# Kernel tuning notes

Hardware: AMD Instinct MI355X
Metric: run time of the kernel (lower is better)

The kernel has to match this reference:

```python
import jax, jax.numpy as jnp
import numpy as np
import math

H = 12
D_MODEL = 768
D_K = D_MODEL // H


def setup_inputs() -> dict:
    key = jax.random.key(0)
    ks = jax.random.split(key, 12)
    B, L = 128, 512
    s = 1.0 / math.sqrt(D_MODEL)
    return {
        "Q": jax.random.normal(ks[0], (B, L, D_MODEL), jnp.float32),
        "K": jax.random.normal(ks[1], (B, L, D_MODEL), jnp.float32),
        "V": jax.random.normal(ks[2], (B, L, D_MODEL), jnp.float32),
        "mask": jax.random.uniform(ks[3], (B, B), jnp.float32),
        "Wq": jax.random.normal(ks[4], (D_MODEL, D_MODEL), jnp.float32) * s,
        "bq": jnp.zeros((D_MODEL,), jnp.float32),
        "Wk": jax.random.normal(ks[5], (D_MODEL, D_MODEL), jnp.float32) * s,
        "bk": jnp.zeros((D_MODEL,), jnp.float32),
        "Wv": jax.random.normal(ks[6], (D_MODEL, D_MODEL), jnp.float32) * s,
        "bv": jnp.zeros((D_MODEL,), jnp.float32),
        "Wo": jax.random.normal(ks[7], (D_MODEL, D_MODEL), jnp.float32) * s,
        "bo": jnp.zeros((D_MODEL,), jnp.float32),
    }


def reference(Q, K, V, mask, Wq, bq, Wk, bk, Wv, bv, Wo, bo):
    nb_q = Q.shape[0]   # nbatches_q = Q.size(0) in the torch code
    nb_kv = K.shape[0]
    # Linear projections then the module's exact reshape/transpose pattern.
    q = (Q @ Wq + bq).reshape(-1, nb_q, H, D_K).swapaxes(1, 2)   # (L, h, B, d_k)
    k = (K @ Wk + bk).reshape(-1, nb_kv, H, D_K).swapaxes(1, 2)  # (L, h, B, d_k)
    v = (V @ Wv + bv).reshape(-1, nb_kv, H, D_K).swapaxes(1, 2)  # (L, h, B, d_k)
    # AttentionAgger: model_dim = d_k -> scale by sqrt(d_k)
    attn = jnp.einsum('lhbd,lhed->lhbe', q, k) / math.sqrt(D_K)  # (L, h, B, B)
    # dual softmax with additive mask bias (mask scaled by its leading dim)
    m = jax.nn.softmax(mask / mask.shape[0], axis=-1)            # (B, B), broadcasts
    attn = jax.nn.softmax(attn, axis=-1) + m
    attn = jax.nn.softmax(attn, axis=-1)
    x = jnp.einsum('lhbe,lhed->lhbd', attn, v)                   # (L, h, B, d_k)
    x = x.swapaxes(1, 2).reshape(-1, nb_q, H * D_K)              # (L, B, d_model)
    return x @ Wo + bo
```

## Files before the change

### kernel.cpp

```cpp
#include <hip/hip_runtime.h>


typedef __attribute__((ext_vector_type(8))) __bf16 bf16x8;
typedef __attribute__((ext_vector_type(4))) __bf16 bf16x4;
typedef __attribute__((ext_vector_type(4))) float f32x4;

#define DM 768
#define LOG2E 1.44269504f

__device__ __forceinline__ unsigned short f2bf(float x) {
  unsigned u = __float_as_uint(x);
  u += 0x7FFFu + ((u >> 16) & 1u);
  return (unsigned short)(u >> 16);
}

__device__ __forceinline__ void gl_lds16(const void* g, void* l) {
  __builtin_amdgcn_global_load_lds(
      (const __attribute__((address_space(1))) unsigned int*)g,
      (__attribute__((address_space(3))) unsigned int*)l, 16, 0, 0);
}

__global__ __launch_bounds__(256) void prep_w(const float* __restrict__ w0,
                                              const float* __restrict__ w1,
                                              const float* __restrict__ w2,
                                              const float* __restrict__ w3,
                                              unsigned short* __restrict__ wt) {
  __shared__ float t[32][33];
  const int op = blockIdx.z;
  const float* w = (op == 0) ? w0 : (op == 1) ? w1 : (op == 2) ? w2 : w3;
  unsigned short* o = wt + (size_t)op * DM * DM;
  const int n0 = blockIdx.x * 32, k0 = blockIdx.y * 32;
  const int tx = threadIdx.x & 31, ty = threadIdx.x >> 5;
#pragma unroll
  for (int r = 0; r < 4; ++r)
    t[r * 8 + ty][tx] = w[(size_t)(k0 + r * 8 + ty) * DM + n0 + tx];
  __syncthreads();
#pragma unroll
  for (int r = 0; r < 4; ++r)
    o[(size_t)(n0 + r * 8 + ty) * DM + k0 + tx] = f2bf(t[tx][r * 8 + ty]);
}

__global__ void prep_m(const float* __restrict__ mask, float* __restrict__ mm) {
  int row = blockIdx.x;
  int t = threadIdx.x;
  float a = mask[row * 128 + t] * (1.0f / 128.0f);
  float b = mask[row * 128 + t + 64] * (1.0f / 128.0f);
  float mx = fmaxf(a, b);
  for (int s = 1; s < 64; s <<= 1) mx = fmaxf(mx, __shfl_xor(mx, s));
  float ea = __expf(a - mx), eb = __expf(b - mx);
  float sum = ea + eb;
  for (int s = 1; s < 64; s <<= 1) sum += __shfl_xor(sum, s);
  float inv = LOG2E / sum;
  mm[row * 128 + t] = ea * inv;
  mm[row * 128 + t + 64] = eb * inv;
}

__global__ __launch_bounds__(256) void convb(const float* __restrict__ in,
                                             unsigned short* __restrict__ out, int n8) {
  int i = blockIdx.x * 256 + threadIdx.x;
  const int stride = gridDim.x * 256;
  for (; i < n8; i += stride) {
    const float4 a = ((const float4*)in)[(size_t)i * 2];
    const float4 b = ((const float4*)in)[(size_t)i * 2 + 1];
    ushort4 lo = {f2bf(a.x), f2bf(a.y), f2bf(a.z), f2bf(a.w)};
    ushort4 hi = {f2bf(b.x), f2bf(b.y), f2bf(b.z), f2bf(b.w)};
    ((ushort4*)out)[(size_t)i * 2] = lo;
    ((ushort4*)out)[(size_t)i * 2 + 1] = hi;
  }
}

__device__ __forceinline__ void stage_tile(const unsigned short* __restrict__ src,
                                           int row0, int kcol, char* slotbase, int tid) {
  const int wid = tid >> 6, lane = tid & 63;
#pragma unroll
  for (int s = 0; s < 2; ++s) {
    const int row = s * 128 + wid * 16 + (lane >> 2);
    const int slot = lane & 3;
    gl_lds16(src + (size_t)(row0 + row) * DM + kcol + ((slot ^ ((row >> 1) & 3)) * 8),
             slotbase + s * 8192 + wid * 1024);
  }
}

template <bool OUT_BF16>
__global__ __launch_bounds__(512, 2) void gemm8(const unsigned short* __restrict__ A,
                                                const unsigned short* __restrict__ Bt,
                                                const float* __restrict__ bias,
                                                void* __restrict__ Outp) {
  __shared__ char smem[131072];
  const int tid = threadIdx.x, lane = tid & 63, wid = tid >> 6;
  const int cl = lane & 15, g = lane >> 4;
  const int wm = wid >> 2, wn = wid & 3;
  const int bid = blockIdx.x;
  const int xcd = bid & 7, bi = bid >> 3;
  const int m0 = (xcd * 32 + bi / 3) * 256;
  const int n0 = (bi % 3) * 256;

  f32x4 acc[8][4] = {};

  auto aslot = [&](int t) { return (char*)smem + (t & 3) * 16384; };
  auto bslot = [&](int t) { return (char*)smem + 65536 + (t & 3) * 16384; };

  auto lda = [&](bf16x8* af, int t, int half) {
#pragma unroll
    for (int mi = 0; mi < 4; ++mi) {
      const int r = wm * 128 + (half * 4 + mi) * 16 + cl;
      af[mi] = *(const bf16x8*)(aslot(t) + r * 64 + ((g ^ ((r >> 1) & 3)) * 16));
    }
  };
  auto ldb = [&](bf16x8* bf, int t) {
#pragma unroll
    for (int ni = 0; ni < 4; ++ni) {
      const int r = wn * 64 + ni * 16 + cl;
      bf[ni] = *(const bf16x8*)(bslot(t) + r * 64 + ((g ^ ((r >> 1) & 3)) * 16));
    }
  };
  auto mfma16 = [&](bf16x8* af, bf16x8* bf, int half) {
    __builtin_amdgcn_s_setprio(1);
#pragma unroll
    for (int mi = 0; mi < 4; ++mi)
#pragma unroll
      for (int ni = 0; ni < 4; ++ni)
        acc[half * 4 + mi][ni] = __builtin_amdgcn_mfma_f32_16x16x32_bf16(
            af[mi], bf[ni], acc[half * 4 + mi][ni], 0, 0, 0);
    __builtin_amdgcn_s_setprio(0);
  };

  auto stg2 = [&](int u) {
    stage_tile(A, m0, u * 32, aslot(u), tid);
    stage_tile(Bt, n0, u * 32, bslot(u), tid);
  };

  stg2(0); stg2(1);
  asm volatile("s_waitcnt vmcnt(0)" ::: "memory");
  __builtin_amdgcn_s_barrier();

  bf16x8 afA[4], af1[4], afB[4], bfA[4], bfB[4];

#pragma unroll 1
  for (int t = 0; t < 12; ++t) {
    const int u = 2 * t;
    if (t < 11) {
      stg2(u + 2); stg2(u + 3);
      asm volatile("s_waitcnt vmcnt(8)" ::: "memory");
    } else {
      asm volatile("s_waitcnt vmcnt(0)" ::: "memory");
    }
    __builtin_amdgcn_s_barrier();
    lda(afA, u, 0); ldb(bfA, u);
    lda(af1, u, 1);
    mfma16(afA, bfA, 0);
    lda(afB, u + 1, 0); ldb(bfB, u + 1);
    mfma16(af1, bfA, 1);
    lda(afA, u + 1, 1);
    mfma16(afB, bfB, 0);
    mfma16(afA, bfB, 1);
    __builtin_amdgcn_s_barrier();
  }

  float bb[4];
#pragma unroll
  for (int ni = 0; ni < 4; ++ni) bb[ni] = bias[n0 + wn * 64 + ni * 16 + cl];
#pragma unroll
  for (int mi = 0; mi < 8; ++mi) {
    const int row = m0 + wm * 128 + mi * 16 + g * 4;
#pragma unroll
    for (int ni = 0; ni < 4; ++ni) {
      const int col = n0 + wn * 64 + ni * 16 + cl;
#pragma unroll
      for (int e = 0; e < 4; ++e) {
        float v = acc[mi][ni][e] + bb[ni];
        if constexpr (OUT_BF16)
          ((unsigned short*)Outp)[(size_t)(row + e) * DM + col] = f2bf(v);
        else
          ((float*)Outp)[(size_t)(row + e) * DM + col] = v;
      }
    }
  }
}

__global__ __launch_bounds__(512) void attn_k(const unsigned short* __restrict__ qp,
                                              const unsigned short* __restrict__ kp,
                                              const unsigned short* __restrict__ vp,
                                              const float* __restrict__ mm,
                                              unsigned short* __restrict__ xout) {
  __shared__ char smem[32768];
  unsigned short* vt = (unsigned short*)(smem + 16384);

  const int tid = threadIdx.x, lane = tid & 63, wid = tid >> 6;
  const int cl = lane & 15, g = lane >> 4;
  const int h = blockIdx.x, l = blockIdx.y;
  const size_t base = (size_t)l * 128 * DM + h * 64;
  const int q = wid * 16 + cl;

#pragma unroll
  for (int p = 0; p < 2; ++p) {
    const int chunk = p * 8 + wid;
    const int row = chunk * 8 + (lane >> 3);
    const int gi = (lane & 7) ^ (row & 7);
    gl_lds16(kp + base + (size_t)row * DM + gi * 8, smem + chunk * 1024);
  }
  if (tid < 256) {
    const int dc = (tid & 7) * 8;
    const int kq = tid >> 3;
    const int pg = (kq ^ ((tid & 7) << 2));
    int4 r0 = *(const int4*)&vp[base + (size_t)(kq * 4 + 0) * DM + dc];
    int4 r1 = *(const int4*)&vp[base + (size_t)(kq * 4 + 1) * DM + dc];
    int4 r2 = *(const int4*)&vp[base + (size_t)(kq * 4 + 2) * DM + dc];
    int4 r3 = *(const int4*)&vp[base + (size_t)(kq * 4 + 3) * DM + dc];
    const unsigned short* u0 = (const unsigned short*)&r0;
    const unsigned short* u1 = (const unsigned short*)&r1;
    const unsigned short* u2 = (const unsigned short*)&r2;
    const unsigned short* u3 = (const unsigned short*)&r3;
#pragma unroll
    for (int j = 0; j < 8; ++j) {
      ushort4 w = {u0[j], u1[j], u2[j], u3[j]};
      *(ushort4*)&vt[(dc + j) * 128 + pg * 4] = w;
    }
  }
  bf16x8 qf[2];
#pragma unroll
  for (int ksr = 0; ksr < 2; ++ksr)
    qf[ksr] = *(const bf16x8*)&qp[base + (size_t)q * DM + ksr * 32 + g * 8];
  __syncthreads();

  f32x4 sacc[8] = {};
  __builtin_amdgcn_s_setprio(1);
#pragma unroll
  for (int ksr = 0; ksr < 2; ++ksr) {
#pragma unroll
    for (int kf = 0; kf < 8; ++kf) {
      const int row = kf * 16 + cl;
      const int gi = (ksr * 4 + g) ^ (row & 7);
      bf16x8 kfr = *(const bf16x8*)(smem + row * 128 + gi * 16);
      sacc[kf] = __builtin_amdgcn_mfma_f32_16x16x32_bf16(kfr, qf[ksr], sacc[kf], 0, 0, 0);
    }
  }
  __builtin_amdgcn_s_setprio(0);
  __syncthreads();

  bf16x4 pk[8];
  {
    float4 mrow[8];
#pragma unroll
    for (int kf = 0; kf < 8; ++kf)
      mrow[kf] = *(const float4*)&mm[q * 128 + kf * 16 + g * 4];
    float sm = 0.f;
#pragma unroll
    for (int kf = 0; kf < 8; ++kf)
#pragma unroll
      for (int e = 0; e < 4; ++e) {
        float p = exp2f(sacc[kf][e] * (0.125f * LOG2E));
        sacc[kf][e] = p;
        sm += p;
      }
    sm += __shfl_xor(sm, 16); sm += __shfl_xor(sm, 32);
    const float inv2e = LOG2E / sm;
    float s2 = 0.f;
#pragma unroll
    for (int kf = 0; kf < 8; ++kf)
#pragma unroll
      for (int e = 0; e < 4; ++e) {
        float p = exp2f(fmaf(sacc[kf][e], inv2e, ((const float*)&mrow[kf])[e]));
        sacc[kf][e] = p;
        s2 += p;
      }
    s2 += __shfl_xor(s2, 16); s2 += __shfl_xor(s2, 32);
    const float inv2 = 1.0f / s2;
#pragma unroll
    for (int kf = 0; kf < 8; ++kf)
      pk[kf] = {(__bf16)(sacc[kf][0] * inv2), (__bf16)(sacc[kf][1] * inv2),
                (__bf16)(sacc[kf][2] * inv2), (__bf16)(sacc[kf][3] * inv2)};
  }

  f32x4 xacc[4] = {};
#pragma unroll
  for (int half = 0; half < 2; ++half) {
#pragma unroll
    for (int kf = 0; kf < 4; ++kf) {
      const int gi = (kf * 4 + g) ^ ((q & 3) << 2);
      *(bf16x4*)(smem + q * 128 + gi * 8) = pk[half * 4 + kf];
    }
    asm volatile("s_waitcnt lgkmcnt(0)" ::: "memory");
    __builtin_amdgcn_sched_barrier(0);
    __builtin_amdgcn_s_setprio(1);
#pragma unroll
    for (int k2 = 0; k2 < 2; ++k2) {
      const int ks2 = half * 2 + k2;
      const int gi = (k2 * 8 + g * 2) ^ ((q & 3) << 2);
      bf16x8 pa = *(const bf16x8*)(smem + q * 128 + gi * 8);
#pragma unroll
      for (int fc = 0; fc < 4; ++fc) {
        const int d = fc * 16 + cl;
        const int pg = (ks2 * 8 + 2 * g) ^ (((d >> 3) & 7) << 2);
        bf16x8 bv = *(const bf16x8*)&vt[d * 128 + pg * 4];
        xacc[fc] = __builtin_amdgcn_mfma_f32_16x16x32_bf16(pa, bv, xacc[fc], 0, 0, 0);
      }
    }
    __builtin_amdgcn_s_setprio(0);
    if (half == 0) {
      asm volatile("s_waitcnt lgkmcnt(0)" ::: "memory");
      __builtin_amdgcn_sched_barrier(0);
    }
  }

#pragma unroll
  for (int fc = 0; fc < 4; ++fc)
#pragma unroll
    for (int e = 0; e < 4; ++e) {
      const int qr = wid * 16 + g * 4 + e;
      __bf16 b = (__bf16)xacc[fc][e];
      unsigned short u;
      __builtin_memcpy(&u, &b, 2);
      xout[base + (size_t)qr * DM + fc * 16 + cl] = u;
    }
}

extern "C" void kernel_launch(void* const* d_in, const int* in_sizes, int n_in,
                              void* d_out, int out_size, void* d_ws, size_t ws_size,
                              hipStream_t stream) {
  (void)in_sizes; (void)n_in; (void)out_size; (void)ws_size;
  const float* Q = (const float*)d_in[0];
  const float* K = (const float*)d_in[1];
  const float* V = (const float*)d_in[2];
  const float* mask = (const float*)d_in[3];
  const float* Wq = (const float*)d_in[4];
  const float* bq = (const float*)d_in[5];
  const float* Wk = (const float*)d_in[6];
  const float* bk = (const float*)d_in[7];
  const float* Wv = (const float*)d_in[8];
  const float* bv = (const float*)d_in[9];
  const float* Wo = (const float*)d_in[10];
  const float* bo = (const float*)d_in[11];

  const size_t NP = (size_t)65536 * DM;

  unsigned short* qp = (unsigned short*)d_out;
  unsigned short* kp = qp + NP;
  unsigned short* S1 = (unsigned short*)d_ws;
  unsigned short* S2 = S1 + NP;
  unsigned short* wt = S2 + NP;
  float* mm = (float*)(wt + (size_t)4 * DM * DM);

  prep_w<<<dim3(24, 24, 4), 256, 0, stream>>>(Wq, Wk, Wv, Wo, wt);
  prep_m<<<dim3(128), 64, 0, stream>>>(mask, mm);

  const int n8 = (int)(NP / 8);
  dim3 g8(768);

  convb<<<dim3(2048), 256, 0, stream>>>(Q, S1, n8);
  gemm8<true><<<g8, 512, 0, stream>>>(S1, wt + 0 * (size_t)DM * DM, bq, qp);
  convb<<<dim3(2048), 256, 0, stream>>>(K, S1, n8);
  gemm8<true><<<g8, 512, 0, stream>>>(S1, wt + 1 * (size_t)DM * DM, bk, kp);
  convb<<<dim3(2048), 256, 0, stream>>>(V, S2, n8);
  gemm8<true><<<g8, 512, 0, stream>>>(S2, wt + 2 * (size_t)DM * DM, bv, S1);

  attn_k<<<dim3(12, 512), 512, 0, stream>>>(qp, kp, S1, mm, S1);

  gemm8<false><<<g8, 512, 0, stream>>>(S1, wt + 3 * (size_t)DM * DM, bo, (float*)d_out);
}
```

Measured before the change: 734.4 us.

## Restructure GEMM main loop into fine-grained 8-phase ping-pong schedule

Replaces the GEMM K-loop, which staged two 32-wide K tiles at a time and then ran four MFMA blocks, with a schedule that handles 64-wide K tiles in two ping-pong LDS buffers. Each iteration is split into eight phases separated by barriers. Each phase interleaves LDS fragment reads, the next tile's global-to-LDS loads for half of A or all of B, and a 4x2x2 MFMA block. The goal is to hide global load latency and LDS reads behind MFMA work, in the style of hipBLASLt's 8-wave ping-pong. The cost is many more barriers per iteration and more complex vmcnt bookkeeping, which could add stalls or ordering hazards.

Result: faster. 667.8 us (-9.1%).

```diff
diff --git a/kernel.cpp b/kernel.cpp
--- a/kernel.cpp
+++ b/kernel.cpp
@@ -18,6 +18,11 @@
   __builtin_amdgcn_global_load_lds(
       (const __attribute__((address_space(1))) unsigned int*)g,
       (__attribute__((address_space(3))) unsigned int*)l, 16, 0, 0);
+}
+
+__device__ __forceinline__ void waitvm(int n) {
+  if (n == 0) asm volatile("s_waitcnt vmcnt(0)" ::: "memory");
+  else        asm volatile("s_waitcnt vmcnt(4)" ::: "memory");
 }
 
 __global__ __launch_bounds__(256) void prep_w(const float* __restrict__ w0,
@@ -69,18 +74,6 @@
   }
 }
 
-__device__ __forceinline__ void stage_tile(const unsigned short* __restrict__ src,
-                                           int row0, int kcol, char* slotbase, int tid) {
-  const int wid = tid >> 6, lane = tid & 63;
-#pragma unroll
-  for (int s = 0; s < 2; ++s) {
-    const int row = s * 128 + wid * 16 + (lane >> 2);
-    const int slot = lane & 3;
-    gl_lds16(src + (size_t)(row0 + row) * DM + kcol + ((slot ^ ((row >> 1) & 3)) * 8),
-             slotbase + s * 8192 + wid * 1024);
-  }
-}
-
 template <bool OUT_BF16>
 __global__ __launch_bounds__(512, 2) void gemm8(const unsigned short* __restrict__ A,
                                                 const unsigned short* __restrict__ Bt,
@@ -97,63 +90,129 @@
 
   f32x4 acc[8][4] = {};
 
-  auto aslot = [&](int t) { return (char*)smem + (t & 3) * 16384; };
-  auto bslot = [&](int t) { return (char*)smem + 65536 + (t & 3) * 16384; };
-
-  auto lda = [&](bf16x8* af, int t, int half) {
+  auto abase = [&](int par, int h, int ss) -> char* {
+    return smem + ((par * 2 + h) * 2 + ss) * 8192;
+  };
+  auto bbase = [&](int par, int h, int ss) -> char* {
+    return smem + 65536 + ((par * 2 + h) * 2 + ss) * 8192;
+  };
+
+  auto stage_u = [&](const unsigned short* src, int rb, int T, int h, char* d0,
+                     char* d1) {
+    const int row = wid * 16 + (lane >> 2);
+    const int slot = lane & 3;
+    const size_t gaddr = (size_t)(rb + h * 128 + row) * DM + T * 64 +
+                         ((slot ^ ((row >> 1) & 3)) * 8);
+    gl_lds16(src + gaddr, d0 + wid * 1024);
+    gl_lds16(src + gaddr + 32, d1 + wid * 1024);
+  };
+
+  auto ldaf = [&](bf16x8 (*af)[2], int par, int f0) {
 #pragma unroll
     for (int mi = 0; mi < 4; ++mi) {
-      const int r = wm * 128 + (half * 4 + mi) * 16 + cl;
-      af[mi] = *(const bf16x8*)(aslot(t) + r * 64 + ((g ^ ((r >> 1) & 3)) * 16));
-    }
-  };
-  auto ldb = [&](bf16x8* bf, int t) {
-#pragma unroll
-    for (int ni = 0; ni < 4; ++ni) {
-      const int r = wn * 64 + ni * 16 + cl;
-      bf[ni] = *(const bf16x8*)(bslot(t) + r * 64 + ((g ^ ((r >> 1) & 3)) * 16));
-    }
-  };
-  auto mfma16 = [&](bf16x8* af, bf16x8* bf, int half) {
+      const int lr = (f0 + mi) * 16 + cl;
+      const int gi = (g ^ ((lr >> 1) & 3)) * 16;
+#pragma unroll
+      for (int ss = 0; ss < 2; ++ss)
+        af[mi][ss] = *(const bf16x8*)(abase(par, wm, ss) + lr * 64 + gi);
+    }
+  };
+  auto ldbf = [&](bf16x8 (*bf)[2], int par, int nf0) {
+#pragma unroll
+    for (int ni = 0; ni < 2; ++ni) {
+      const int lr = (wn & 1) * 64 + (nf0 + ni) * 16 + cl;
+      const int gi = (g ^ ((lr >> 1) & 3)) * 16;
+#pragma unroll
+      for (int ss = 0; ss < 2; ++ss)
+        bf[ni][ss] = *(const bf16x8*)(bbase(par, wn >> 1, ss) + lr * 64 + gi);
+    }
+  };
+  auto mf16 = [&](bf16x8 (*af)[2], bf16x8 (*bf)[2], int f0, int nf0) {
     __builtin_amdgcn_s_setprio(1);
 #pragma unroll
-    for (int mi = 0; mi < 4; ++mi)
-#pragma unroll
-      for (int ni = 0; ni < 4; ++ni)
-        acc[half * 4 + mi][ni] = __builtin_amdgcn_mfma_f32_16x16x32_bf16(
-            af[mi], bf[ni], acc[half * 4 + mi][ni], 0, 0, 0);
+    for (int ss = 0; ss < 2; ++ss)
+#pragma unroll
+      for (int mi = 0; mi < 4; ++mi)
+#pragma unroll
+        for (int ni = 0; ni < 2; ++ni)
+          acc[f0 + mi][nf0 + ni] = __builtin_amdgcn_mfma_f32_16x16x32_bf16(
+              af[mi][ss], bf[ni][ss], acc[f0 + mi][nf0 + ni], 0, 0, 0);
     __builtin_amdgcn_s_setprio(0);
   };
 
-  auto stg2 = [&](int u) {
-    stage_tile(A, m0, u * 32, aslot(u), tid);
-    stage_tile(Bt, n0, u * 32, bslot(u), tid);
-  };
-
-  stg2(0); stg2(1);
-  asm volatile("s_waitcnt vmcnt(0)" ::: "memory");
+#pragma unroll
+  for (int T = 0; T < 2; ++T)
+#pragma unroll
+    for (int h = 0; h < 2; ++h) {
+      stage_u(A, m0, T, h, abase(T, h, 0), abase(T, h, 1));
+      stage_u(Bt, n0, T, h, bbase(T, h, 0), bbase(T, h, 1));
+    }
+  waitvm(0);
   __builtin_amdgcn_s_barrier();
 
-  bf16x8 afA[4], af1[4], afB[4], bfA[4], bfB[4];
-
 #pragma unroll 1
-  for (int t = 0; t < 12; ++t) {
-    const int u = 2 * t;
-    if (t < 11) {
-      stg2(u + 2); stg2(u + 3);
-      asm volatile("s_waitcnt vmcnt(8)" ::: "memory");
+  for (int i = 0; i < 6; ++i) {
+    const int T1 = 2 * i + 1;
+    const bool sA = (i >= 1);
+    const bool sF = (i <= 4);
+    bf16x8 afA[4][2], afB[4][2], bfA[2][2], bfB[2][2];
+
+    ldaf(afA, 0, 0);
+    ldbf(bfA, 0, 0);
+    if (sA) stage_u(A, m0, T1, 0, abase(1, 0, 0), abase(1, 0, 1));
+    __builtin_amdgcn_s_barrier();
+    mf16(afA, bfA, 0, 0);
+    __builtin_amdgcn_s_barrier();
+
+    ldaf(afB, 0, 4);
+    if (sA) stage_u(A, m0, T1, 1, abase(1, 1, 0), abase(1, 1, 1));
+    __builtin_amdgcn_s_barrier();
+    mf16(afB, bfA, 4, 0);
+    __builtin_amdgcn_s_barrier();
+
+    ldbf(bfB, 0, 2);
+    __builtin_amdgcn_s_barrier();
+    mf16(afB, bfB, 4, 2);
+    __builtin_amdgcn_s_barrier();
+
+    ldaf(afA, 0, 0);
+    if (sF) {
+      stage_u(Bt, n0, T1 + 1, 0, bbase(0, 0, 0), bbase(0, 0, 1));
+      stage_u(Bt, n0, T1 + 1, 1, bbase(0, 1, 0), bbase(0, 1, 1));
+      waitvm(4);
     } else {
-      asm volatile("s_waitcnt vmcnt(0)" ::: "memory");
-    }
-    __builtin_amdgcn_s_barrier();
-    lda(afA, u, 0); ldb(bfA, u);
-    lda(af1, u, 1);
-    mfma16(afA, bfA, 0);
-    lda(afB, u + 1, 0); ldb(bfB, u + 1);
-    mfma16(af1, bfA, 1);
-    lda(afA, u + 1, 1);
-    mfma16(afB, bfB, 0);
-    mfma16(afA, bfB, 1);
+      waitvm(0);
+    }
+    __builtin_amdgcn_s_barrier();
+    mf16(afA, bfB, 0, 2);
+    __builtin_amdgcn_s_barrier();
+
+    ldaf(afA, 1, 0);
+    ldbf(bfA, 1, 0);
+    if (sF) stage_u(A, m0, T1 + 1, 0, abase(0, 0, 0), abase(0, 0, 1));
+    __builtin_amdgcn_s_barrier();
+    mf16(afA, bfA, 0, 0);
+    __builtin_amdgcn_s_barrier();
+
+    ldaf(afB, 1, 4);
+    if (sF) stage_u(A, m0, T1 + 1, 1, abase(0, 1, 0), abase(0, 1, 1));
+    __builtin_amdgcn_s_barrier();
+    mf16(afB, bfA, 4, 0);
+    __builtin_amdgcn_s_barrier();
+
+    ldbf(bfB, 1, 2);
+    __builtin_amdgcn_s_barrier();
+    mf16(afB, bfB, 4, 2);
+    __builtin_amdgcn_s_barrier();
+
+    ldaf(afA, 1, 0);
+    if (sF) {
+      stage_u(Bt, n0, T1 + 2, 0, bbase(1, 0, 0), bbase(1, 0, 1));
+      stage_u(Bt, n0, T1 + 2, 1, bbase(1, 1, 0), bbase(1, 1, 1));
+      waitvm(4);
+    }
+    __builtin_amdgcn_s_barrier();
+    mf16(afA, bfB, 0, 2);
     __builtin_amdgcn_s_barrier();
   }
 
```
